# Optimization experiments

Measured on AMD Instinct MI355X. Metric: run time of the kernel, lower is better.

The kernel has to match this reference:

```python
import jax, jax.numpy as jnp
import numpy as np

N_NODES = 500_000
N_FEAT = 125          # embedding dim; cat with pos(3) -> 128
HIDDEN = 128
OUT_DIM = 64
N_TYPES = 100
N_GRAPHS = 4096


def setup_inputs() -> dict:
    key = jax.random.key(0)
    ks = jax.random.split(key, 10)
    pos = jax.random.normal(ks[0], (N_NODES, 3), dtype=jnp.float32)
    z = jax.random.randint(ks[1], (N_NODES,), 0, N_TYPES)
    batch = jnp.sort(jax.random.randint(ks[2], (N_NODES,), 0, N_GRAPHS))
    emb = jax.random.normal(ks[3], (N_TYPES, N_FEAT), dtype=jnp.float32)
    s1 = 1.0 / np.sqrt(N_FEAT + 3)
    s2 = 1.0 / np.sqrt(HIDDEN)
    W1 = jax.random.normal(ks[4], (N_FEAT + 3, HIDDEN), dtype=jnp.float32) * s1
    b1 = jnp.zeros((HIDDEN,), dtype=jnp.float32)
    W2 = jax.random.normal(ks[5], (HIDDEN, HIDDEN), dtype=jnp.float32) * s2
    b2 = jnp.zeros((HIDDEN,), dtype=jnp.float32)
    W3 = jax.random.normal(ks[6], (HIDDEN, OUT_DIM), dtype=jnp.float32) * s2
    b3 = jnp.zeros((OUT_DIM,), dtype=jnp.float32)
    return {"pos": pos, "z": z, "batch": batch, "emb": emb,
            "W1": W1, "b1": b1, "W2": W2, "b2": b2, "W3": W3, "b3": b3}


def reference(pos, z, batch, emb, W1, b1, W2, b2, W3, b3):
    # embed node types and concat with 3D positions  -> [N, 128]
    x = jnp.concatenate([pos, emb[z]], axis=-1)
    # two equivariant-transformer layers (per-node transform) + relu
    x = jax.nn.relu(x @ W1 + b1)   # [N, H]
    x = jax.nn.relu(x @ W2 + b2)   # [N, H]
    # output head
    x = x @ W3 + b3                # [N, O]
    # global mean pool per graph
    s = jax.ops.segment_sum(x, batch, num_segments=N_GRAPHS)                    # [G, O]
    cnt = jax.ops.segment_sum(jnp.ones((x.shape[0], 1), x.dtype), batch,
                              num_segments=N_GRAPHS)                            # [G, 1]
    return s / jnp.maximum(cnt, 1.0)
```

## Files before the change

kernel.cpp:

```cpp
#include <hip/hip_runtime.h>
#include <hip/hip_bf16.h>

#define N_NODES 500000
#define N_FEAT 125
#define HID 128
#define OUTD 64
#define N_GRAPHS 4096
#define N_TYPES 100
#define WTILE 32
#define NTILES32 (N_NODES / WTILE)
#define NBLOCKS 256
#define NWAVES 8
#define WPAD 136

typedef float f32x4 __attribute__((ext_vector_type(4)));
typedef short s16x8 __attribute__((ext_vector_type(8)));

#define OFF_T 0
#define SZ_T (N_TYPES * WPAD * 2)
#define OFF_W2 (OFF_T + SZ_T)
#define OFF_W3 (OFF_W2 + HID * WPAD * 2)
#define OFF_B2 (OFF_W3 + OUTD * WPAD * 2)
#define OFF_SCR (OFF_B2 + HID * 4)
#define SCR_BYTES (WTILE * WPAD * 2)
#define LDS_BYTES (OFF_SCR + NWAVES * SCR_BYTES)

#define WS_GSUM 0
#define WS_GCNT ((size_t)N_GRAPHS * OUTD * 4)
#define WS_T    (WS_GCNT + (size_t)N_GRAPHS * 4)
#define WS_ZERO WS_T

__device__ __forceinline__ unsigned short f2bf(float f) {
  union { float f; unsigned u; } v; v.f = f;
  unsigned r = v.u + 0x7FFFu + ((v.u >> 16) & 1u);
  return (unsigned short)(r >> 16);
}
__device__ __forceinline__ float bf2f(unsigned short u) {
  union { unsigned u; float f; } v; v.u = ((unsigned)u) << 16;
  return v.f;
}
__device__ __forceinline__ unsigned pk2bf(float a, float b) {
  __hip_bfloat162 h = __float22bfloat162_rn(float2{a, b});
  union { __hip_bfloat162 h; unsigned u; } v; v.h = h;
  return v.u;
}

__device__ __forceinline__ void wavefence() {
  __builtin_amdgcn_sched_barrier(0);
  __builtin_amdgcn_wave_barrier();
  __builtin_amdgcn_sched_barrier(0);
}

extern "C" __global__ void gnn_prep(const float* __restrict__ emb,
                                    const float* __restrict__ W1,
                                    const float* __restrict__ b1,
                                    unsigned short* __restrict__ Tg)
{
  const int g = blockIdx.x, j = threadIdx.x;
  float acc = b1[j];
  const float* er = emb + g * N_FEAT;
  for (int k = 0; k < N_FEAT; ++k)
    acc = fmaf(er[k], W1[(3 + k) * HID + j], acc);
  Tg[g * HID + j] = f2bf(acc);
}

extern "C" __global__ void __launch_bounds__(512, 2)
gnn_main(const float* __restrict__ pos, const int* __restrict__ z,
         const int* __restrict__ batch, const unsigned short* __restrict__ Tg,
         const float* __restrict__ W1, const float* __restrict__ W2,
         const float* __restrict__ b2, const float* __restrict__ W3,
         float* __restrict__ gsum, int* __restrict__ gcnt)
{
  extern __shared__ char lds[];
  unsigned short* Tl  = (unsigned short*)(lds + OFF_T);
  unsigned short* w2t = (unsigned short*)(lds + OFF_W2);
  unsigned short* w3t = (unsigned short*)(lds + OFF_W3);
  float* bias2 = (float*)(lds + OFF_B2);

  const int t = threadIdx.x;

  for (int i = t; i < N_TYPES * HID; i += 512) {
    int g = i >> 7, f = i & 127;
    Tl[g * WPAD + f] = Tg[i];
  }
  for (int i = t; i < HID * HID; i += 512) {
    int k = i >> 7, n = i & 127;
    w2t[n * WPAD + k] = f2bf(W2[i]);
  }
  for (int i = t; i < HID * OUTD; i += 512) {
    int k = i >> 6, n = i & 63;
    w3t[n * WPAD + k] = f2bf(W3[i]);
  }
  if (t < HID) bias2[t] = b2[t];

  const int wave = t >> 6, lane = t & 63, quad = lane >> 4, l15 = lane & 15;
  unsigned short* xs = (unsigned short*)(lds + OFF_SCR + wave * SCR_BYTES);

  float w1r[3][4][8];
  #pragma unroll
  for (int c = 0; c < 3; ++c)
    #pragma unroll
    for (int k = 0; k < 4; ++k)
      #pragma unroll
      for (int j = 0; j < 8; ++j)
        w1r[c][k][j] = W1[c * HID + k * 32 + quad * 8 + j];

  __syncthreads();

  const int gwave = blockIdx.x * NWAVES + wave;

  for (int tile = gwave; tile < NTILES32; tile += NBLOCKS * NWAVES) {
    const int base = tile * WTILE;

    const int id0 = batch[base + l15];
    const int id1 = batch[base + 16 + l15];

    s16x8 a[2][4];
    #pragma unroll
    for (int m = 0; m < 2; ++m) {
      const int node = base + m * 16 + l15;
      const int zi = z[node];
      const float px = pos[node * 3], py = pos[node * 3 + 1], pz = pos[node * 3 + 2];
      const unsigned short* Tr = Tl + zi * WPAD;
      #pragma unroll
      for (int k = 0; k < 4; ++k) {
        s16x8 tf = *(const s16x8*)(Tr + k * 32 + quad * 8);
        s16x8 fr;
        #pragma unroll
        for (int j = 0; j < 8; j += 2) {
          float v0 = bf2f((unsigned short)tf[j])
                   + px * w1r[0][k][j] + py * w1r[1][k][j] + pz * w1r[2][k][j];
          float v1 = bf2f((unsigned short)tf[j + 1])
                   + px * w1r[0][k][j + 1] + py * w1r[1][k][j + 1] + pz * w1r[2][k][j + 1];
          ((unsigned*)&fr)[j >> 1] = pk2bf(fmaxf(v0, 0.f), fmaxf(v1, 0.f));
        }
        a[m][k] = fr;
      }
    }

    f32x4 acc[8][2] = {};
    __builtin_amdgcn_s_setprio(1);
    #pragma unroll
    for (int oi = 0; oi < 8; ++oi)
      #pragma unroll
      for (int k = 0; k < 4; ++k) {
        s16x8 w = *(const s16x8*)(w2t + (oi * 16 + l15) * WPAD + k * 32 + quad * 8);
        acc[oi][0] = __builtin_amdgcn_mfma_f32_16x16x32_bf16(w, a[0][k], acc[oi][0], 0, 0, 0);
        acc[oi][1] = __builtin_amdgcn_mfma_f32_16x16x32_bf16(w, a[1][k], acc[oi][1], 0, 0, 0);
      }
    __builtin_amdgcn_s_setprio(0);
    #pragma unroll
    for (int oi = 0; oi < 8; ++oi) {
      const int f0 = oi * 16 + quad * 4;
      f32x4 bv = *(const f32x4*)(bias2 + f0);
      #pragma unroll
      for (int m = 0; m < 2; ++m) {
        unsigned lo = pk2bf(fmaxf(acc[oi][m][0] + bv[0], 0.f),
                            fmaxf(acc[oi][m][1] + bv[1], 0.f));
        unsigned hi = pk2bf(fmaxf(acc[oi][m][2] + bv[2], 0.f),
                            fmaxf(acc[oi][m][3] + bv[3], 0.f));
        *(uint2*)(xs + (m * 16 + l15) * WPAD + f0) = uint2{lo, hi};
      }
    }
    wavefence();
    #pragma unroll
    for (int m = 0; m < 2; ++m)
      #pragma unroll
      for (int k = 0; k < 4; ++k)
        a[m][k] = *(const s16x8*)(xs + (m * 16 + l15) * WPAD + k * 32 + quad * 8);
    wavefence();

    f32x4 acc3[4][2] = {};
    __builtin_amdgcn_s_setprio(1);
    #pragma unroll
    for (int oi = 0; oi < 4; ++oi)
      #pragma unroll
      for (int k = 0; k < 4; ++k) {
        s16x8 w = *(const s16x8*)(w3t + (oi * 16 + l15) * WPAD + k * 32 + quad * 8);
        acc3[oi][0] = __builtin_amdgcn_mfma_f32_16x16x32_bf16(w, a[0][k], acc3[oi][0], 0, 0, 0);
        acc3[oi][1] = __builtin_amdgcn_mfma_f32_16x16x32_bf16(w, a[1][k], acc3[oi][1], 0, 0, 0);
      }
    __builtin_amdgcn_s_setprio(0);

    {
      int done = 0;
      while (done < 32) {
        const int g = __builtin_amdgcn_readfirstlane(batch[base + done]);
        const bool m0 = (id0 == g), m1 = (id1 == g);
        float red[4][4];
        #pragma unroll
        for (int oi = 0; oi < 4; ++oi)
          #pragma unroll
          for (int r = 0; r < 4; ++r)
            red[oi][r] = (m0 ? acc3[oi][0][r] : 0.f) + (m1 ? acc3[oi][1][r] : 0.f);
        #pragma unroll
        for (int s = 1; s <= 8; s <<= 1)
          #pragma unroll
          for (int oi = 0; oi < 4; ++oi)
            #pragma unroll
            for (int r = 0; r < 4; ++r)
              red[oi][r] += __shfl_xor(red[oi][r], s, 64);
        const int cnt = (int)((__popcll(__ballot(m0)) + __popcll(__ballot(m1))) >> 2);
        if (l15 == 0) {
          #pragma unroll
          for (int oi = 0; oi < 4; ++oi)
            #pragma unroll
            for (int r = 0; r < 4; ++r)
              atomicAdd(&gsum[g * OUTD + oi * 16 + quad * 4 + r], red[oi][r]);
        }
        if (lane == 0) atomicAdd(&gcnt[g], cnt);
        done += cnt;
      }
    }
  }
}

extern "C" __global__ void gnn_finalize(const float* __restrict__ gsum,
                                        const int* __restrict__ gcnt,
                                        const float* __restrict__ b3,
                                        float* __restrict__ out)
{
  int i = blockIdx.x * 256 + threadIdx.x;
  if (i < N_GRAPHS * OUTD) {
    int g = i >> 6, o = i & 63;
    int c = gcnt[g];
    out[i] = (c > 0) ? (gsum[i] / (float)c + b3[o]) : 0.f;
  }
}

extern "C" void kernel_launch(void* const* d_in, const int* in_sizes, int n_in,
                              void* d_out, int out_size, void* d_ws, size_t ws_size,
                              hipStream_t stream) {
  const float* pos  = (const float*)d_in[0];
  const int*   z    = (const int*)d_in[1];
  const int*   batch= (const int*)d_in[2];
  const float* emb  = (const float*)d_in[3];
  const float* W1   = (const float*)d_in[4];
  const float* b1   = (const float*)d_in[5];
  const float* W2   = (const float*)d_in[6];
  const float* b2   = (const float*)d_in[7];
  const float* W3   = (const float*)d_in[8];
  const float* b3   = (const float*)d_in[9];

  float* gsum = (float*)d_ws;
  int*   gcnt = (int*)((char*)d_ws + WS_GCNT);
  unsigned short* Tg = (unsigned short*)((char*)d_ws + WS_T);

  hipMemsetAsync(d_ws, 0, WS_ZERO, stream);

  hipLaunchKernelGGL(gnn_prep, dim3(N_TYPES), dim3(HID), 0, stream, emb, W1, b1, Tg);

  hipFuncSetAttribute((const void*)gnn_main,
                      hipFuncAttributeMaxDynamicSharedMemorySize, LDS_BYTES);
  hipLaunchKernelGGL(gnn_main, dim3(NBLOCKS), dim3(512), LDS_BYTES, stream,
                     pos, z, batch, Tg, W1, W2, b2, W3, gsum, gcnt);
  hipLaunchKernelGGL(gnn_finalize, dim3((N_GRAPHS * OUTD + 255) / 256), dim3(256), 0, stream,
                     gsum, gcnt, b3, (float*)d_out);
}
```

Baseline: 147.7 us.

## Raise occupancy by dropping LDS scratch, moving W1 to LDS, fusing memset into prep

Removes the per-wave LDS scratch used to transpose layer-2 output and instead reshuffles the packed bf16 activations across lanes with ds_bpermute. W1 position weights move from 96 registers per thread into LDS, and launch bounds rise to 4 blocks per CU with twice as many blocks. The workspace memset is folded into the prep kernel, and the per-segment graph id comes from readlane on already-loaded ids instead of a global load. Together these aim at higher occupancy and fewer launches and loads, at the cost of extra bpermute and LDS reads per tile and tighter register limits that could spill.

```diff
diff --git a/kernel.cpp b/kernel.cpp
--- a/kernel.cpp
+++ b/kernel.cpp
@@ -9,7 +9,7 @@
 #define N_TYPES 100
 #define WTILE 32
 #define NTILES32 (N_NODES / WTILE)
-#define NBLOCKS 256
+#define NBLOCKS 512
 #define NWAVES 8
 #define WPAD 136
 
@@ -21,14 +21,14 @@
 #define OFF_W2 (OFF_T + SZ_T)
 #define OFF_W3 (OFF_W2 + HID * WPAD * 2)
 #define OFF_B2 (OFF_W3 + OUTD * WPAD * 2)
-#define OFF_SCR (OFF_B2 + HID * 4)
-#define SCR_BYTES (WTILE * WPAD * 2)
-#define LDS_BYTES (OFF_SCR + NWAVES * SCR_BYTES)
+#define OFF_W1 (OFF_B2 + HID * 4)
+#define LDS_BYTES (OFF_W1 + 3 * HID * 4)
 
 #define WS_GSUM 0
 #define WS_GCNT ((size_t)N_GRAPHS * OUTD * 4)
 #define WS_T    (WS_GCNT + (size_t)N_GRAPHS * 4)
 #define WS_ZERO WS_T
+#define WS_ZERO_V4 (WS_ZERO / 16)
 
 __device__ __forceinline__ unsigned short f2bf(float f) {
   union { float f; unsigned u; } v; v.f = f;
@@ -45,26 +45,27 @@
   return v.u;
 }
 
-__device__ __forceinline__ void wavefence() {
-  __builtin_amdgcn_sched_barrier(0);
-  __builtin_amdgcn_wave_barrier();
-  __builtin_amdgcn_sched_barrier(0);
-}
-
 extern "C" __global__ void gnn_prep(const float* __restrict__ emb,
                                     const float* __restrict__ W1,
                                     const float* __restrict__ b1,
-                                    unsigned short* __restrict__ Tg)
+                                    unsigned short* __restrict__ Tg,
+                                    f32x4* __restrict__ wsz)
 {
-  const int g = blockIdx.x, j = threadIdx.x;
-  float acc = b1[j];
-  const float* er = emb + g * N_FEAT;
-  for (int k = 0; k < N_FEAT; ++k)
-    acc = fmaf(er[k], W1[(3 + k) * HID + j], acc);
-  Tg[g * HID + j] = f2bf(acc);
-}
-
-extern "C" __global__ void __launch_bounds__(512, 2)
+  const int j = threadIdx.x;
+  const int tid = blockIdx.x * 128 + j;
+  for (int i = tid; i < WS_ZERO_V4; i += 256 * 128)
+    wsz[i] = (f32x4){0.f, 0.f, 0.f, 0.f};
+  const int g = blockIdx.x;
+  if (g < N_TYPES) {
+    float acc = b1[j];
+    const float* er = emb + g * N_FEAT;
+    for (int k = 0; k < N_FEAT; ++k)
+      acc = fmaf(er[k], W1[(3 + k) * HID + j], acc);
+    Tg[g * HID + j] = f2bf(acc);
+  }
+}
+
+extern "C" __global__ void __launch_bounds__(512, 4)
 gnn_main(const float* __restrict__ pos, const int* __restrict__ z,
          const int* __restrict__ batch, const unsigned short* __restrict__ Tg,
          const float* __restrict__ W1, const float* __restrict__ W2,
@@ -76,6 +77,7 @@
   unsigned short* w2t = (unsigned short*)(lds + OFF_W2);
   unsigned short* w3t = (unsigned short*)(lds + OFF_W3);
   float* bias2 = (float*)(lds + OFF_B2);
+  float* w1l   = (float*)(lds + OFF_W1);
 
   const int t = threadIdx.x;
 
@@ -92,18 +94,12 @@
     w3t[n * WPAD + k] = f2bf(W3[i]);
   }
   if (t < HID) bias2[t] = b2[t];
+  if (t < 3 * HID) w1l[t] = W1[t];
 
   const int wave = t >> 6, lane = t & 63, quad = lane >> 4, l15 = lane & 15;
-  unsigned short* xs = (unsigned short*)(lds + OFF_SCR + wave * SCR_BYTES);
-
-  float w1r[3][4][8];
-  #pragma unroll
-  for (int c = 0; c < 3; ++c)
-    #pragma unroll
-    for (int k = 0; k < 4; ++k)
-      #pragma unroll
-      for (int j = 0; j < 8; ++j)
-        w1r[c][k][j] = W1[c * HID + k * 32 + quad * 8 + j];
+  const bool hi32 = (lane >= 32);
+  const int A0 = ((((lane >> 4) & 1) << 5) + l15) << 2;
+  const int A1 = A0 + 64;
 
   __syncthreads();
 
@@ -115,23 +111,34 @@
     const int id0 = batch[base + l15];
     const int id1 = batch[base + 16 + l15];
 
-    s16x8 a[2][4];
+    float px[2], py[2], pz[2];
+    const unsigned short* Tr[2];
     #pragma unroll
     for (int m = 0; m < 2; ++m) {
       const int node = base + m * 16 + l15;
       const int zi = z[node];
-      const float px = pos[node * 3], py = pos[node * 3 + 1], pz = pos[node * 3 + 2];
-      const unsigned short* Tr = Tl + zi * WPAD;
-      #pragma unroll
-      for (int k = 0; k < 4; ++k) {
-        s16x8 tf = *(const s16x8*)(Tr + k * 32 + quad * 8);
+      px[m] = pos[node * 3]; py[m] = pos[node * 3 + 1]; pz[m] = pos[node * 3 + 2];
+      Tr[m] = Tl + zi * WPAD;
+    }
+    s16x8 a[2][4];
+    #pragma unroll
+    for (int k = 0; k < 4; ++k) {
+      float w1s[3][8];
+      #pragma unroll
+      for (int c = 0; c < 3; ++c) {
+        *(f32x4*)&w1s[c][0] = *(const f32x4*)(w1l + c * HID + k * 32 + quad * 8);
+        *(f32x4*)&w1s[c][4] = *(const f32x4*)(w1l + c * HID + k * 32 + quad * 8 + 4);
+      }
+      #pragma unroll
+      for (int m = 0; m < 2; ++m) {
+        s16x8 tf = *(const s16x8*)(Tr[m] + k * 32 + quad * 8);
         s16x8 fr;
         #pragma unroll
         for (int j = 0; j < 8; j += 2) {
           float v0 = bf2f((unsigned short)tf[j])
-                   + px * w1r[0][k][j] + py * w1r[1][k][j] + pz * w1r[2][k][j];
+                   + px[m] * w1s[0][j] + py[m] * w1s[1][j] + pz[m] * w1s[2][j];
           float v1 = bf2f((unsigned short)tf[j + 1])
-                   + px * w1r[0][k][j + 1] + py * w1r[1][k][j + 1] + pz * w1r[2][k][j + 1];
+                   + px[m] * w1s[0][j + 1] + py[m] * w1s[1][j + 1] + pz[m] * w1s[2][j + 1];
           ((unsigned*)&fr)[j >> 1] = pk2bf(fmaxf(v0, 0.f), fmaxf(v1, 0.f));
         }
         a[m][k] = fr;
@@ -149,26 +156,35 @@
         acc[oi][1] = __builtin_amdgcn_mfma_f32_16x16x32_bf16(w, a[1][k], acc[oi][1], 0, 0, 0);
       }
     __builtin_amdgcn_s_setprio(0);
+
+    unsigned P[8][2][2];
     #pragma unroll
     for (int oi = 0; oi < 8; ++oi) {
       const int f0 = oi * 16 + quad * 4;
       f32x4 bv = *(const f32x4*)(bias2 + f0);
       #pragma unroll
       for (int m = 0; m < 2; ++m) {
-        unsigned lo = pk2bf(fmaxf(acc[oi][m][0] + bv[0], 0.f),
+        P[oi][m][0] = pk2bf(fmaxf(acc[oi][m][0] + bv[0], 0.f),
                             fmaxf(acc[oi][m][1] + bv[1], 0.f));
-        unsigned hi = pk2bf(fmaxf(acc[oi][m][2] + bv[2], 0.f),
+        P[oi][m][1] = pk2bf(fmaxf(acc[oi][m][2] + bv[2], 0.f),
                             fmaxf(acc[oi][m][3] + bv[3], 0.f));
-        *(uint2*)(xs + (m * 16 + l15) * WPAD + f0) = uint2{lo, hi};
-      }
-    }
-    wavefence();
+      }
+    }
+
     #pragma unroll
     for (int m = 0; m < 2; ++m)
       #pragma unroll
-      for (int k = 0; k < 4; ++k)
-        a[m][k] = *(const s16x8*)(xs + (m * 16 + l15) * WPAD + k * 32 + quad * 8);
-    wavefence();
+      for (int kb = 0; kb < 4; ++kb) {
+        s16x8 fr;
+        #pragma unroll
+        for (int j2 = 0; j2 < 4; ++j2) {
+          const int addr = (j2 < 2) ? A0 : A1;
+          int t0 = __builtin_amdgcn_ds_bpermute(addr, (int)P[2 * kb][m][j2 & 1]);
+          int t1 = __builtin_amdgcn_ds_bpermute(addr, (int)P[2 * kb + 1][m][j2 & 1]);
+          ((int*)&fr)[j2] = hi32 ? t1 : t0;
+        }
+        a[m][kb] = fr;
+      }
 
     f32x4 acc3[4][2] = {};
     __builtin_amdgcn_s_setprio(1);
@@ -185,7 +201,8 @@
     {
       int done = 0;
       while (done < 32) {
-        const int g = __builtin_amdgcn_readfirstlane(batch[base + done]);
+        const int srcv = (done < 16) ? id0 : id1;
+        const int g = __builtin_amdgcn_readlane(srcv, done & 15);
         const bool m0 = (id0 == g), m1 = (id1 == g);
         float red[4][4];
         #pragma unroll
@@ -246,9 +263,8 @@
   int*   gcnt = (int*)((char*)d_ws + WS_GCNT);
   unsigned short* Tg = (unsigned short*)((char*)d_ws + WS_T);
 
-  hipMemsetAsync(d_ws, 0, WS_ZERO, stream);
-
-  hipLaunchKernelGGL(gnn_prep, dim3(N_TYPES), dim3(HID), 0, stream, emb, W1, b1, Tg);
+  hipLaunchKernelGGL(gnn_prep, dim3(256), dim3(HID), 0, stream,
+                     emb, W1, b1, Tg, (f32x4*)d_ws);
 
   hipFuncSetAttribute((const void*)gnn_main,
                       hipFuncAttributeMaxDynamicSharedMemorySize, LDS_BYTES);
```

Result: slower. 164.5 us (+11.4%).
